# Performance work log

Hardware: AMD Instinct MI355X
Metric: run time of the kernel (lower is better)

Reference implementation:

```python
import jax, jax.numpy as jnp
import numpy as np

B, S, E = 2, 2048, 2048
H, KVH, D = 16, 4, 128
GROUPS = H // KVH
WINDOW = 1024
CAP = 50.0
ROPE_BASE = 10000.0
RMS_EPS = 1e-6
LN_EPS = 1e-5

def setup_inputs() -> dict:
    key = jax.random.key(0)
    ks = jax.random.split(key, 5)
    return {
        "x": jax.random.normal(ks[0], (B, S, E), jnp.float32),
        "Wq": jax.random.normal(ks[1], (E, E), jnp.float32) * (1.0 / np.sqrt(E)),
        "Wk": jax.random.normal(ks[2], (KVH * D, E), jnp.float32) * (1.0 / np.sqrt(E)),
        "Wv": jax.random.normal(ks[3], (KVH * D, E), jnp.float32) * (1.0 / np.sqrt(E)),
        "Wo": jax.random.normal(ks[4], (E, E), jnp.float32) * (1.0 / np.sqrt(E * H)),
        "q_norm_w": jnp.ones((D,), jnp.float32),
        "k_norm_w": jnp.ones((D,), jnp.float32),
        "ln_gamma": jnp.ones((E,), jnp.float32),
        "ln_beta": jnp.zeros((E,), jnp.float32),
    }

def _rmsnorm(t, w):
    # normalize over last (head) dim
    var = jnp.mean(jnp.square(t), axis=-1, keepdims=True)
    return t * jax.lax.rsqrt(var + RMS_EPS) * w

def _rope(t):
    # t: [B, h, S, D]; rotate-half RoPE
    half = D // 2
    inv_freq = 1.0 / (ROPE_BASE ** (jnp.arange(0, D, 2, dtype=jnp.float32) / D))  # [D/2]
    ang = jnp.arange(S, dtype=jnp.float32)[:, None] * inv_freq[None, :]  # [S, D/2]
    cos = jnp.concatenate([jnp.cos(ang), jnp.cos(ang)], axis=-1)  # [S, D]
    sin = jnp.concatenate([jnp.sin(ang), jnp.sin(ang)], axis=-1)
    t1, t2 = t[..., :half], t[..., half:]
    rot = jnp.concatenate([-t2, t1], axis=-1)
    return t * cos + rot * sin

def reference(x, Wq, Wk, Wv, Wo, q_norm_w, k_norm_w, ln_gamma, ln_beta):
    b, s, _ = x.shape
    q = (x @ Wq.T).reshape(b, s, H, D).transpose(0, 2, 1, 3)    # [B,H,S,D]
    k = (x @ Wk.T).reshape(b, s, KVH, D).transpose(0, 2, 1, 3)  # [B,KVH,S,D]
    v = (x @ Wv.T).reshape(b, s, KVH, D).transpose(0, 2, 1, 3)
    # QK-RMSNorm (Gemma/PaLM2 style), then RoPE
    q = _rope(_rmsnorm(q, q_norm_w))
    k = _rope(_rmsnorm(k, k_norm_w))
    # GQA: repeat KV heads to match query heads
    k = jnp.repeat(k, GROUPS, axis=1)  # [B,H,S,D]
    v = jnp.repeat(v, GROUPS, axis=1)
    scores = jnp.einsum('bhqd,bhkd->bhqk', q, k) / jnp.sqrt(jnp.asarray(D, x.dtype))
    # tanh logit softcap (Gemma2)
    scores = CAP * jnp.tanh(scores / CAP)
    # causal + sliding-window mask: attend to j with 0 <= i-j < WINDOW
    i = jnp.arange(s)[:, None]
    j = jnp.arange(s)[None, :]
    mask = (j <= i) & ((i - j) < WINDOW)  # [S,S]
    neg = jnp.finfo(scores.dtype).min
    scores = jnp.where(mask[None, None], scores, neg)
    attn = jax.nn.softmax(scores, axis=-1)
    out = jnp.einsum('bhqk,bhkd->bhqd', attn, v)  # [B,H,S,D]
    out = out.transpose(0, 2, 1, 3).reshape(b, s, E) @ Wo.T
    # residual + LayerNorm (post-norm)
    y = x + out
    mu = jnp.mean(y, axis=-1, keepdims=True)
    var = jnp.var(y, axis=-1, keepdims=True)
    return (y - mu) * jax.lax.rsqrt(var + LN_EPS) * ln_gamma + ln_beta
```

## Files before the change

### kernel.cpp

```cpp
#include <hip/hip_runtime.h>
#include <stdint.h>

typedef __attribute__((ext_vector_type(8))) short short8;
typedef __attribute__((ext_vector_type(4))) float f32x4;
typedef unsigned short u16;
typedef unsigned int u32;

#define NTOK 4096
#define E 2048
#define S 2048
#define NH 16
#define NKVH 4
#define HD 128
#define NQKV 3072

__device__ __forceinline__ float bf2f(u16 u) {
    return __uint_as_float(((u32)u) << 16);
}
__device__ __forceinline__ u16 f2bf(float f) {
    u32 u = __float_as_uint(f);
    u32 r = (u + 0x7fffu + ((u >> 16) & 1u)) >> 16;
    return (u16)r;
}
__device__ __forceinline__ void gload_lds16(const u16* g, u16* l) {
    __builtin_amdgcn_global_load_lds(
        (const __attribute__((address_space(1))) unsigned int*)(g),
        (__attribute__((address_space(3))) unsigned int*)(l), 16, 0, 0);
}

__global__ void cast5(const float* __restrict__ x, const float* __restrict__ wq,
                      const float* __restrict__ wk, const float* __restrict__ wv,
                      const float* __restrict__ wo,
                      u16* __restrict__ xb, u16* __restrict__ wqkvb,
                      u16* __restrict__ wob) {
    int i = blockIdx.x * 256 + threadIdx.x;
    const float* s; u16* d; int rel;
    if (i < 2097152)      { s = x;  d = xb;  rel = i; }
    else if (i < 3145728) { s = wq; d = wqkvb; rel = i - 2097152; }
    else if (i < 3407872) { s = wk; d = wqkvb + 4194304; rel = i - 3145728; }
    else if (i < 3670016) { s = wv; d = wqkvb + 5242880; rel = i - 3407872; }
    else                  { s = wo; d = wob; rel = i - 3670016; }
    float4 v = *(const float4*)(s + (size_t)rel * 4);
    ushort4 o;
    o.x = f2bf(v.x); o.y = f2bf(v.y); o.z = f2bf(v.z); o.w = f2bf(v.w);
    *(ushort4*)(d + (size_t)rel * 4) = o;
}

#define LADDR(row, ko) ((row) * 64 + ((ko) ^ (((row) & 7) << 3)))

__device__ __forceinline__ void stageA(u16* lds, const u16* g, int ldsrow0,
                                       int g0, int g1, int kt, int K, int tid) {
    const int rr = tid >> 3;
    const int chunk = (tid & 7) ^ (rr & 7);
    const int w8 = (tid >> 6) * 8;
    gload_lds16(g + (size_t)(g0 + rr) * K + kt + chunk * 8,
                lds + (ldsrow0 + w8) * 64);
    gload_lds16(g + (size_t)(g1 + rr) * K + kt + chunk * 8,
                lds + (ldsrow0 + 64 + w8) * 64);
}
__device__ __forceinline__ void stageB(u16* lds, const u16* g, int ldsrow0,
                                       int b0, int b1, int kt, int K, int tid) {
    const int rr = tid >> 3;
    const int grow = (rr & 31) | ((rr & 32) << 1);
    const int chunk = (tid & 7) ^ (rr & 7);
    const int w8 = (tid >> 6) * 8;
    gload_lds16(g + (size_t)(b0 + grow) * K + kt + chunk * 8,
                lds + (ldsrow0 + w8) * 64);
    gload_lds16(g + (size_t)(b1 + grow) * K + kt + chunk * 8,
                lds + (ldsrow0 + 64 + w8) * 64);
}

#define GSB   __builtin_amdgcn_sched_barrier(0)
#define GBAR  __builtin_amdgcn_s_barrier()
#define LGKM0 do { asm volatile("s_waitcnt lgkmcnt(0)" ::: "memory"); GSB; } while (0)
#define MIDBAR do { GSB; GBAR; LGKM0; } while (0)
#define ENDBAR do { __builtin_amdgcn_s_setprio(0); GSB; GBAR; } while (0)

__global__ __launch_bounds__(512, 2)
void gemm8p(const u16* __restrict__ A, const u16* __restrict__ Bt,
            float* __restrict__ C, int M, int N, int K) {
    __shared__ u16 As[2 * 16384];
    __shared__ u16 Bs[2 * 16384];
    const int tid = threadIdx.x;
    const int w = tid >> 6, lane = tid & 63;
    const int lr = lane & 15, quad = lane >> 4;
    const int qo = quad * 8;
    const int wm = (w >> 2) * 128, wn = (w & 3) * 64;
    const int wmh = (w >> 2) * 64, wnq = (w & 3) * 32;

    const int nbx = N >> 8;
    int wg = blockIdx.x;
    {
        const int nwg = gridDim.x;
        const int q = nwg >> 3, r = nwg & 7;
        const int xcd = wg & 7, loc = wg >> 3;
        wg = (xcd < r ? xcd * (q + 1) : r * (q + 1) + (xcd - r) * q) + loc;
    }
    const int n0 = (wg % nbx) << 8;
    const int m0 = (wg / nbx) << 8;

    const u16* gA = A + (size_t)m0 * K;
    const u16* gB = Bt + (size_t)n0 * K;
    const int nt = K >> 6;

    f32x4 acc[8][4];
#pragma unroll
    for (int mi = 0; mi < 8; mi++)
#pragma unroll
        for (int ni = 0; ni < 4; ni++)
            acc[mi][ni] = (f32x4){0.f, 0.f, 0.f, 0.f};

    short8 alo[4][2], ahi[4][2], blo[2][2], bhi[2][2];

    stageA(As, gA, 0, 0, 128, 0, K, tid);
    stageB(Bs, gB, 0, 0, 128, 0, K, tid);
    stageB(Bs, gB, 128, 32, 160, 0, K, tid);
    stageA(As, gA, 128, 64, 192, 0, K, tid);
    if (nt > 1) {
        stageA(As + 16384, gA, 0, 0, 128, 64, K, tid);
        stageB(Bs + 16384, gB, 0, 0, 128, 64, K, tid);
        stageB(Bs + 16384, gB, 128, 32, 160, 64, K, tid);
        asm volatile("s_waitcnt vmcnt(6)" ::: "memory");
    } else {
        asm volatile("s_waitcnt vmcnt(0)" ::: "memory");
    }
    GSB; GBAR;

    for (int t = 0; t < nt; ++t) {
        const int pb = t & 1;
        u16* Ap = As + pb * 16384;
        u16* Bp = Bs + pb * 16384;
        u16* An = As + (pb ^ 1) * 16384;
        const int kt1 = (t + 1) << 6, kt2 = (t + 2) << 6;

#pragma unroll
        for (int mi = 0; mi < 4; mi++)
#pragma unroll
            for (int kk = 0; kk < 2; kk++)
                alo[mi][kk] = *(const short8*)&Ap[LADDR(wmh + mi * 16 + lr, kk * 32 + qo)];
#pragma unroll
        for (int ni = 0; ni < 2; ni++)
#pragma unroll
            for (int kk = 0; kk < 2; kk++)
                blo[ni][kk] = *(const short8*)&Bp[LADDR(wnq + ni * 16 + lr, kk * 32 + qo)];
        if (t + 1 < nt) stageA(An, gA, 128, 64, 192, kt1, K, tid);
        MIDBAR;
        __builtin_amdgcn_s_setprio(1);
#pragma unroll
        for (int mi = 0; mi < 4; mi++)
#pragma unroll
            for (int ni = 0; ni < 2; ni++)
#pragma unroll
                for (int kk = 0; kk < 2; kk++)
                    acc[mi][ni] = __builtin_amdgcn_mfma_f32_16x16x32_bf16(
                        alo[mi][kk], blo[ni][kk], acc[mi][ni], 0, 0, 0);
        ENDBAR;

#pragma unroll
        for (int ni = 0; ni < 2; ni++)
#pragma unroll
            for (int kk = 0; kk < 2; kk++)
                bhi[ni][kk] = *(const short8*)&Bp[LADDR(128 + wnq + ni * 16 + lr, kk * 32 + qo)];
        if (t + 2 < nt) stageA(Ap, gA, 0, 0, 128, kt2, K, tid);
        MIDBAR;
        __builtin_amdgcn_s_setprio(1);
#pragma unroll
        for (int mi = 0; mi < 4; mi++)
#pragma unroll
            for (int ni = 0; ni < 2; ni++)
#pragma unroll
                for (int kk = 0; kk < 2; kk++)
                    acc[mi][ni + 2] = __builtin_amdgcn_mfma_f32_16x16x32_bf16(
                        alo[mi][kk], bhi[ni][kk], acc[mi][ni + 2], 0, 0, 0);
        ENDBAR;

#pragma unroll
        for (int mi = 0; mi < 4; mi++)
#pragma unroll
            for (int kk = 0; kk < 2; kk++)
                ahi[mi][kk] = *(const short8*)&Ap[LADDR(128 + wmh + mi * 16 + lr, kk * 32 + qo)];
        if (t + 2 < nt) stageB(Bp, gB, 0, 0, 128, kt2, K, tid);
        MIDBAR;
        __builtin_amdgcn_s_setprio(1);
#pragma unroll
        for (int mi = 0; mi < 4; mi++)
#pragma unroll
            for (int ni = 0; ni < 2; ni++)
#pragma unroll
                for (int kk = 0; kk < 2; kk++)
                    acc[mi + 4][ni + 2] = __builtin_amdgcn_mfma_f32_16x16x32_bf16(
                        ahi[mi][kk], bhi[ni][kk], acc[mi + 4][ni + 2], 0, 0, 0);
        ENDBAR;

        if (t + 2 < nt) stageB(Bp, gB, 128, 32, 160, kt2, K, tid);
        __builtin_amdgcn_s_setprio(1);
#pragma unroll
        for (int mi = 0; mi < 4; mi++)
#pragma unroll
            for (int ni = 0; ni < 2; ni++)
#pragma unroll
                for (int kk = 0; kk < 2; kk++)
                    acc[mi + 4][ni] = __builtin_amdgcn_mfma_f32_16x16x32_bf16(
                        ahi[mi][kk], blo[ni][kk], acc[mi + 4][ni], 0, 0, 0);
        __builtin_amdgcn_s_setprio(0);
        if (t + 2 >= nt) {
            asm volatile("s_waitcnt vmcnt(0)" ::: "memory");
        } else {
            asm volatile("s_waitcnt vmcnt(6)" ::: "memory");
        }
        GSB; GBAR;
    }

#pragma unroll
    for (int mi = 0; mi < 8; mi++)
#pragma unroll
        for (int ni = 0; ni < 4; ni++) {
            const int row = m0 + wm + mi * 16 + quad * 4;
            const int col = n0 + wn + ni * 16 + lr;
            f32x4 v = acc[mi][ni];
            C[(size_t)(row + 0) * N + col] = v[0];
            C[(size_t)(row + 1) * N + col] = v[1];
            C[(size_t)(row + 2) * N + col] = v[2];
            C[(size_t)(row + 3) * N + col] = v[3];
        }
}

__global__ __launch_bounds__(256)
void rmsrope2(const float* __restrict__ qkv,
              const float* __restrict__ qw, const float* __restrict__ kw,
              u16* __restrict__ qdst, u16* __restrict__ kdst) {
    int p = blockIdx.x * 4 + (threadIdx.x >> 6);
    int lane = threadIdx.x & 63;
    const float* src; const float* w; u16* dst; int HH;
    if (p < NTOK * NH) { src = qkv; w = qw; dst = qdst; HH = NH; }
    else { p -= NTOK * NH; src = qkv + 2048; w = kw; dst = kdst; HH = NKVH; }
    int n = p / HH;
    int h = p - n * HH;
    int b = n >> 11;
    int s = n & 2047;
    const float* row = src + (size_t)n * NQKV + h * HD;
    float t1 = row[lane];
    float t2 = row[lane + 64];
    float ss = t1 * t1 + t2 * t2;
#pragma unroll
    for (int o = 1; o < 64; o <<= 1) ss += __shfl_xor(ss, o);
    float r = rsqrtf(ss * (1.f / 128.f) + 1e-6f);
    float a1 = t1 * r * w[lane];
    float a2 = t2 * r * w[lane + 64];
    float freq = expf(lane * -0.14391156831212787f);
    float ang = (float)s * freq;
    float sn, cs;
    sincosf(ang, &sn, &cs);
    float o1 = a1 * cs - a2 * sn;
    float o2 = a2 * cs + a1 * sn;
    size_t base = (((size_t)(b * HH + h)) * S + s) * HD;
    dst[base + lane] = f2bf(o1);
    dst[base + 64 + lane] = f2bf(o2);
}

#define LDT 65
__global__ __launch_bounds__(256)
void vtrans(const float* __restrict__ src, u16* __restrict__ dst) {
    __shared__ u16 Ts[128 * LDT];
    const int t = threadIdx.x;
    const int s0 = blockIdx.x * 64;
    const int kh = blockIdx.y;
    const int b = blockIdx.z;
    const float* base = src + ((size_t)(b * S + s0)) * NQKV + 2560 + kh * HD;
#pragma unroll
    for (int i = 0; i < 8; i++) {
        int idx = i * 256 + t;
        int r = idx >> 5, c4 = (idx & 31) * 4;
        float4 v = *(const float4*)(base + (size_t)r * NQKV + c4);
        Ts[(c4 + 0) * LDT + r] = f2bf(v.x);
        Ts[(c4 + 1) * LDT + r] = f2bf(v.y);
        Ts[(c4 + 2) * LDT + r] = f2bf(v.z);
        Ts[(c4 + 3) * LDT + r] = f2bf(v.w);
    }
    __syncthreads();
    u16* obase = dst + ((size_t)(b * NKVH + kh) * HD) * S + s0;
#pragma unroll
    for (int i = 0; i < 4; i++) {
        int idx = i * 256 + t;
        int d = idx >> 3, s8 = (idx & 7) * 8;
        const u16* row = &Ts[d * LDT + s8];
        short8 o;
#pragma unroll
        for (int j = 0; j < 8; j++) o[j] = (short)row[j];
        *(short8*)(obase + (size_t)d * S + s8) = o;
    }
}

#define KSX(key, cb) ((key) * 128 + ((((cb) ^ ((key) & 15))) * 8))
#define VSX(d, cb)   ((d) * 64 + ((((cb) ^ ((d) & 7))) * 8))
#define PSX(row, cb) ((row) * 64 + ((((cb) ^ ((row) & 7))) * 8))
#define QBLK 64

__global__ __launch_bounds__(256, 4)
void attn_mfma(const u16* __restrict__ qa, const u16* __restrict__ ka,
               const u16* __restrict__ vt, u16* __restrict__ out) {
    __shared__ u16 Ks[64 * 128];
    __shared__ u16 Vs[128 * 64];
    __shared__ u16 Ps[64 * 64];
    const int tid = threadIdx.x;
    const int w = tid >> 6, lane = tid & 63;
    const int lr = lane & 15, quad = lane >> 4;
    const int hb = blockIdx.x;
    const int h = hb >> 1, b = hb & 1;
    const int kh = h >> 2;
    const int qt = (int)(gridDim.y - 1) - blockIdx.y;
    const int q0 = qt * QBLK;
    const int qg0 = q0 + w * 16;

    const float KQK = 0.0051006974f;
    const float KP  = -144.26950408889634f;

    short8 qf[4];
    {
        const u16* qrow = qa + (((size_t)(b * NH + h)) * S + qg0 + lr) * HD;
#pragma unroll
        for (int c = 0; c < 4; c++)
            qf[c] = *(const short8*)(qrow + c * 32 + quad * 8);
    }

    f32x4 O[8];
#pragma unroll
    for (int dt = 0; dt < 8; dt++) O[dt] = (f32x4){0.f, 0.f, 0.f, 0.f};
    float l[4] = {0.f, 0.f, 0.f, 0.f};

    const u16* kbase0 = ka + (((size_t)(b * NKVH + kh)) * S) * HD;
    const u16* vtbase0 = vt + ((size_t)(b * NKVH + kh) * HD) * S;

    const int jt0 = (q0 >= 1024) ? (q0 - 1024) : 0;
    const int jtend = q0;
    const int qmin = qg0, qmax = qg0 + 15;

    for (int jt = jt0; jt <= jtend; jt += 64) {
        const u16* kbase = kbase0 + (size_t)jt * HD;
        const u16* vtbase = vtbase0 + jt;
        __syncthreads();
#pragma unroll
        for (int i = 0; i < 4; i++) {
            int idx = i * 256 + tid;
            int key = idx >> 4, cbk = (idx & 15) ^ (key & 15);
            gload_lds16(kbase + (size_t)key * HD + cbk * 8,
                        &Ks[(i * 256 + w * 64) * 8]);
            int dd = idx >> 3, cbv = (idx & 7) ^ (dd & 7);
            gload_lds16(vtbase + (size_t)dd * S + cbv * 8,
                        &Vs[(i * 256 + w * 64) * 8]);
        }
        __syncthreads();

        u16* Pw = &Ps[w * 16 * 64];
        bool any = false;

#pragma unroll
        for (int kt = 0; kt < 4; kt++) {
            const int keymin = jt + kt * 16;
            bool need = (keymin <= qmax) && (keymin + 15 >= qmin - 1023);
            bool full = (keymin + 15 <= qmin) && (keymin >= qmax - 1023);
            if (need) {
                any = true;
                f32x4 a = (f32x4){0.f, 0.f, 0.f, 0.f};
#pragma unroll
                for (int c = 0; c < 4; c++) {
                    short8 kf = *(const short8*)(&Ks[KSX(kt * 16 + lr, 4 * c + quad)]);
                    a = __builtin_amdgcn_mfma_f32_16x16x32_bf16(qf[c], kf, a, 0, 0, 0);
                }
#pragma unroll
                for (int r = 0; r < 4; r++) {
                    float t = __builtin_amdgcn_exp2f(a[r] * KQK);
                    float p = __builtin_amdgcn_exp2f(
                        KP * __builtin_amdgcn_rcpf(t + 1.f));
                    if (!full) {
                        int rel = keymin + lr - (qg0 + quad * 4 + r);
                        bool valid = (rel <= 0) && (rel > -1024);
                        p = valid ? p : 0.f;
                    }
                    l[r] += p;
                    Pw[PSX(quad * 4 + r, kt * 2 + (lr >> 3)) + (lr & 7)] =
                        (u16)(__float_as_uint(p) >> 16);
                }
            } else {
#pragma unroll
                for (int r = 0; r < 4; r++)
                    Pw[PSX(quad * 4 + r, kt * 2 + (lr >> 3)) + (lr & 7)] = 0;
            }
        }

        if (any) {
#pragma unroll
            for (int c2 = 0; c2 < 2; c2++) {
                short8 pf = *(const short8*)(&Pw[PSX(lr, c2 * 4 + quad)]);
#pragma unroll
                for (int dt = 0; dt < 8; dt++) {
                    short8 vf = *(const short8*)(&Vs[VSX(dt * 16 + lr, c2 * 4 + quad)]);
                    O[dt] = __builtin_amdgcn_mfma_f32_16x16x32_bf16(pf, vf, O[dt], 0, 0, 0);
                }
            }
        }
    }

#pragma unroll
    for (int r = 0; r < 4; r++) {
        l[r] += __shfl_xor(l[r], 1);
        l[r] += __shfl_xor(l[r], 2);
        l[r] += __shfl_xor(l[r], 4);
        l[r] += __shfl_xor(l[r], 8);
    }
#pragma unroll
    for (int r = 0; r < 4; r++) {
        float inv = 1.f / l[r];
        u16* orow = out + ((size_t)(b * S + qg0 + quad * 4 + r)) * E + h * HD;
#pragma unroll
        for (int dt = 0; dt < 8; dt++)
            orow[dt * 16 + lr] = f2bf(O[dt][r] * inv);
    }
}

__global__ __launch_bounds__(256)
void ln_kernel(const float* __restrict__ x, const float* __restrict__ pr,
               const float* __restrict__ g, const float* __restrict__ be,
               float* __restrict__ out) {
    int n = blockIdx.x;
    int tid = threadIdx.x;
    const float* xr = x + (size_t)n * E;
    const float* p = pr + (size_t)n * E;
    float y[8];
    float s = 0.f, ss = 0.f;
#pragma unroll
    for (int i = 0; i < 2; i++) {
        float4 a = *(const float4*)(xr + tid * 8 + i * 4);
        float4 b = *(const float4*)(p + tid * 8 + i * 4);
        float v0 = a.x + b.x, v1 = a.y + b.y, v2 = a.z + b.z, v3 = a.w + b.w;
        y[i * 4 + 0] = v0; y[i * 4 + 1] = v1; y[i * 4 + 2] = v2; y[i * 4 + 3] = v3;
        s += v0 + v1 + v2 + v3;
        ss += v0 * v0 + v1 * v1 + v2 * v2 + v3 * v3;
    }
#pragma unroll
    for (int o = 1; o < 64; o <<= 1) {
        s += __shfl_xor(s, o);
        ss += __shfl_xor(ss, o);
    }
    __shared__ float r0[4], r1[4];
    int w = tid >> 6;
    if ((tid & 63) == 0) { r0[w] = s; r1[w] = ss; }
    __syncthreads();
    s = r0[0] + r0[1] + r0[2] + r0[3];
    ss = r1[0] + r1[1] + r1[2] + r1[3];
    float mu = s * (1.f / 2048.f);
    float var = ss * (1.f / 2048.f) - mu * mu;
    float rs = rsqrtf(var + 1e-5f);
    float* orow = out + (size_t)n * E;
#pragma unroll
    for (int i = 0; i < 8; i++) {
        int c = tid * 8 + i;
        orow[c] = (y[i] - mu) * rs * g[c] + be[c];
    }
}

extern "C" void kernel_launch(void* const* d_in, const int* in_sizes, int n_in,
                              void* d_out, int out_size, void* d_ws, size_t ws_size,
                              hipStream_t stream) {
    (void)in_sizes; (void)n_in; (void)out_size; (void)ws_size;
    const float* x   = (const float*)d_in[0];
    const float* Wq  = (const float*)d_in[1];
    const float* Wk  = (const float*)d_in[2];
    const float* Wv  = (const float*)d_in[3];
    const float* Wo  = (const float*)d_in[4];
    const float* qnw = (const float*)d_in[5];
    const float* knw = (const float*)d_in[6];
    const float* lng = (const float*)d_in[7];
    const float* lnb = (const float*)d_in[8];
    float* out = (float*)d_out;

    char* ws = (char*)d_ws;
    size_t off = 0;
    auto alloc = [&](size_t bytes) -> char* {
        char* pp = ws + off;
        off = (off + bytes + 255) & ~(size_t)255;
        return pp;
    };
    u16*  xb     = (u16*)alloc((size_t)NTOK * E * 2);
    u16*  Wqkvb  = (u16*)alloc((size_t)NQKV * E * 2);
    u16*  Wob    = (u16*)alloc((size_t)E * E * 2);
    float* qkvraw= (float*)alloc((size_t)NTOK * NQKV * 4);
    u16*  qaa    = (u16*)alloc((size_t)NTOK * E * 2);
    u16*  kaa    = (u16*)alloc((size_t)NTOK * 512 * 2);
    u16*  vtt    = (u16*)alloc((size_t)NTOK * 512 * 2);
    u16*  attn_o = xb;
    float* proj  = qkvraw;

    cast5<<<dim3(18432), 256, 0, stream>>>(x, Wq, Wk, Wv, Wo, xb, Wqkvb, Wob);

    gemm8p<<<dim3((NTOK / 256) * (NQKV / 256)), 512, 0, stream>>>(
        xb, Wqkvb, qkvraw, NTOK, NQKV, E);

    rmsrope2<<<dim3((NTOK * NH + NTOK * NKVH) / 4), 256, 0, stream>>>(
        qkvraw, qnw, knw, qaa, kaa);
    vtrans<<<dim3(S / 64, NKVH, 2), 256, 0, stream>>>(qkvraw, vtt);

    attn_mfma<<<dim3(NH * 2, S / QBLK), 256, 0, stream>>>(qaa, kaa, vtt, attn_o);

    gemm8p<<<dim3((NTOK / 256) * (E / 256)), 512, 0, stream>>>(
        attn_o, Wob, proj, NTOK, E, E);

    ln_kernel<<<dim3(NTOK), 256, 0, stream>>>(x, proj, lng, lnb, out);
}
```

Baseline: 339.6 us.

## Split-K the output projection GEMM and merge rmsrope/vtrans into one launch

The output projection GEMM (4096x2048x2048) is split along K into two halves, doubling the grid from 128 to 256 workgroups so that more of the device's compute units are occupied. The two partial results are written to separate buffers and summed in the LayerNorm kernel, which now reads an extra fp32 matrix. Separately, the RMSNorm+RoPE and V-transpose kernels are fused into a single launch, dispatched by block index, to save one launch. The trade-off is extra global traffic for the second partial buffer, and the fused kernel now reserves transpose shared memory for every block.

```diff
diff --git a/kernel.cpp b/kernel.cpp
--- a/kernel.cpp
+++ b/kernel.cpp
@@ -78,7 +78,7 @@
 
 __global__ __launch_bounds__(512, 2)
 void gemm8p(const u16* __restrict__ A, const u16* __restrict__ Bt,
-            float* __restrict__ C, int M, int N, int K) {
+            float* __restrict__ C, int M, int N, int K, int ksz, int nsplit) {
     __shared__ u16 As[2 * 16384];
     __shared__ u16 Bs[2 * 16384];
     const int tid = threadIdx.x;
@@ -96,12 +96,15 @@
         const int xcd = wg & 7, loc = wg >> 3;
         wg = (xcd < r ? xcd * (q + 1) : r * (q + 1) + (xcd - r) * q) + loc;
     }
+    int split = 0;
+    if (nsplit == 2) { split = wg & 1; wg >>= 1; }
     const int n0 = (wg % nbx) << 8;
     const int m0 = (wg / nbx) << 8;
 
-    const u16* gA = A + (size_t)m0 * K;
-    const u16* gB = Bt + (size_t)n0 * K;
-    const int nt = K >> 6;
+    const u16* gA = A + (size_t)m0 * K + split * ksz;
+    const u16* gB = Bt + (size_t)n0 * K + split * ksz;
+    C += (size_t)split * M * N;
+    const int nt = ksz >> 6;
 
     f32x4 acc[8][4];
 #pragma unroll
@@ -225,69 +228,70 @@
         }
 }
 
+#define LDT 65
+#define RMSBLKS 20480
 __global__ __launch_bounds__(256)
-void rmsrope2(const float* __restrict__ qkv,
-              const float* __restrict__ qw, const float* __restrict__ kw,
-              u16* __restrict__ qdst, u16* __restrict__ kdst) {
-    int p = blockIdx.x * 4 + (threadIdx.x >> 6);
-    int lane = threadIdx.x & 63;
-    const float* src; const float* w; u16* dst; int HH;
-    if (p < NTOK * NH) { src = qkv; w = qw; dst = qdst; HH = NH; }
-    else { p -= NTOK * NH; src = qkv + 2048; w = kw; dst = kdst; HH = NKVH; }
-    int n = p / HH;
-    int h = p - n * HH;
-    int b = n >> 11;
-    int s = n & 2047;
-    const float* row = src + (size_t)n * NQKV + h * HD;
-    float t1 = row[lane];
-    float t2 = row[lane + 64];
-    float ss = t1 * t1 + t2 * t2;
-#pragma unroll
-    for (int o = 1; o < 64; o <<= 1) ss += __shfl_xor(ss, o);
-    float r = rsqrtf(ss * (1.f / 128.f) + 1e-6f);
-    float a1 = t1 * r * w[lane];
-    float a2 = t2 * r * w[lane + 64];
-    float freq = expf(lane * -0.14391156831212787f);
-    float ang = (float)s * freq;
-    float sn, cs;
-    sincosf(ang, &sn, &cs);
-    float o1 = a1 * cs - a2 * sn;
-    float o2 = a2 * cs + a1 * sn;
-    size_t base = (((size_t)(b * HH + h)) * S + s) * HD;
-    dst[base + lane] = f2bf(o1);
-    dst[base + 64 + lane] = f2bf(o2);
-}
-
-#define LDT 65
-__global__ __launch_bounds__(256)
-void vtrans(const float* __restrict__ src, u16* __restrict__ dst) {
+void prep(const float* __restrict__ qkv,
+          const float* __restrict__ qw, const float* __restrict__ kw,
+          u16* __restrict__ qdst, u16* __restrict__ kdst, u16* __restrict__ vdst) {
     __shared__ u16 Ts[128 * LDT];
-    const int t = threadIdx.x;
-    const int s0 = blockIdx.x * 64;
-    const int kh = blockIdx.y;
-    const int b = blockIdx.z;
-    const float* base = src + ((size_t)(b * S + s0)) * NQKV + 2560 + kh * HD;
-#pragma unroll
-    for (int i = 0; i < 8; i++) {
-        int idx = i * 256 + t;
-        int r = idx >> 5, c4 = (idx & 31) * 4;
-        float4 v = *(const float4*)(base + (size_t)r * NQKV + c4);
-        Ts[(c4 + 0) * LDT + r] = f2bf(v.x);
-        Ts[(c4 + 1) * LDT + r] = f2bf(v.y);
-        Ts[(c4 + 2) * LDT + r] = f2bf(v.z);
-        Ts[(c4 + 3) * LDT + r] = f2bf(v.w);
-    }
-    __syncthreads();
-    u16* obase = dst + ((size_t)(b * NKVH + kh) * HD) * S + s0;
-#pragma unroll
-    for (int i = 0; i < 4; i++) {
-        int idx = i * 256 + t;
-        int d = idx >> 3, s8 = (idx & 7) * 8;
-        const u16* row = &Ts[d * LDT + s8];
-        short8 o;
-#pragma unroll
-        for (int j = 0; j < 8; j++) o[j] = (short)row[j];
-        *(short8*)(obase + (size_t)d * S + s8) = o;
+    if (blockIdx.x < RMSBLKS) {
+        int p = blockIdx.x * 4 + (threadIdx.x >> 6);
+        int lane = threadIdx.x & 63;
+        const float* src; const float* w; u16* dst; int HH;
+        if (p < NTOK * NH) { src = qkv; w = qw; dst = qdst; HH = NH; }
+        else { p -= NTOK * NH; src = qkv + 2048; w = kw; dst = kdst; HH = NKVH; }
+        int n = p / HH;
+        int h = p - n * HH;
+        int b = n >> 11;
+        int s = n & 2047;
+        const float* row = src + (size_t)n * NQKV + h * HD;
+        float t1 = row[lane];
+        float t2 = row[lane + 64];
+        float ss = t1 * t1 + t2 * t2;
+#pragma unroll
+        for (int o = 1; o < 64; o <<= 1) ss += __shfl_xor(ss, o);
+        float r = rsqrtf(ss * (1.f / 128.f) + 1e-6f);
+        float a1 = t1 * r * w[lane];
+        float a2 = t2 * r * w[lane + 64];
+        float freq = expf(lane * -0.14391156831212787f);
+        float ang = (float)s * freq;
+        float sn, cs;
+        sincosf(ang, &sn, &cs);
+        float o1 = a1 * cs - a2 * sn;
+        float o2 = a2 * cs + a1 * sn;
+        size_t base = (((size_t)(b * HH + h)) * S + s) * HD;
+        dst[base + lane] = f2bf(o1);
+        dst[base + 64 + lane] = f2bf(o2);
+    } else {
+        const int idx = blockIdx.x - RMSBLKS;
+        const int t = threadIdx.x;
+        const int s0 = (idx & 31) * 64;
+        const int kh = (idx >> 5) & 3;
+        const int b = idx >> 7;
+        const float* base = qkv + ((size_t)(b * S + s0)) * NQKV + 2560 + kh * HD;
+#pragma unroll
+        for (int i = 0; i < 8; i++) {
+            int ii = i * 256 + t;
+            int r = ii >> 5, c4 = (ii & 31) * 4;
+            float4 v = *(const float4*)(base + (size_t)r * NQKV + c4);
+            Ts[(c4 + 0) * LDT + r] = f2bf(v.x);
+            Ts[(c4 + 1) * LDT + r] = f2bf(v.y);
+            Ts[(c4 + 2) * LDT + r] = f2bf(v.z);
+            Ts[(c4 + 3) * LDT + r] = f2bf(v.w);
+        }
+        __syncthreads();
+        u16* obase = vdst + ((size_t)(b * NKVH + kh) * HD) * S + s0;
+#pragma unroll
+        for (int i = 0; i < 4; i++) {
+            int ii = i * 256 + t;
+            int d = ii >> 3, s8 = (ii & 7) * 8;
+            const u16* row = &Ts[d * LDT + s8];
+            short8 o;
+#pragma unroll
+            for (int j = 0; j < 8; j++) o[j] = (short)row[j];
+            *(short8*)(obase + (size_t)d * S + s8) = o;
+        }
     }
 }
 
@@ -420,19 +424,25 @@
 
 __global__ __launch_bounds__(256)
 void ln_kernel(const float* __restrict__ x, const float* __restrict__ pr,
+               const float* __restrict__ pr2,
                const float* __restrict__ g, const float* __restrict__ be,
                float* __restrict__ out) {
     int n = blockIdx.x;
     int tid = threadIdx.x;
     const float* xr = x + (size_t)n * E;
     const float* p = pr + (size_t)n * E;
+    const float* p2 = pr2 + (size_t)n * E;
     float y[8];
     float s = 0.f, ss = 0.f;
 #pragma unroll
     for (int i = 0; i < 2; i++) {
         float4 a = *(const float4*)(xr + tid * 8 + i * 4);
         float4 b = *(const float4*)(p + tid * 8 + i * 4);
-        float v0 = a.x + b.x, v1 = a.y + b.y, v2 = a.z + b.z, v3 = a.w + b.w;
+        float c = 0.f;
+        float4 cc = *(const float4*)(p2 + tid * 8 + i * 4);
+        (void)c;
+        float v0 = a.x + b.x + cc.x, v1 = a.y + b.y + cc.y;
+        float v2 = a.z + b.z + cc.z, v3 = a.w + b.w + cc.w;
         y[i * 4 + 0] = v0; y[i * 4 + 1] = v1; y[i * 4 + 2] = v2; y[i * 4 + 3] = v3;
         s += v0 + v1 + v2 + v3;
         ss += v0 * v0 + v1 * v1 + v2 * v2 + v3 * v3;
@@ -494,16 +504,15 @@
     cast5<<<dim3(18432), 256, 0, stream>>>(x, Wq, Wk, Wv, Wo, xb, Wqkvb, Wob);
 
     gemm8p<<<dim3((NTOK / 256) * (NQKV / 256)), 512, 0, stream>>>(
-        xb, Wqkvb, qkvraw, NTOK, NQKV, E);
-
-    rmsrope2<<<dim3((NTOK * NH + NTOK * NKVH) / 4), 256, 0, stream>>>(
-        qkvraw, qnw, knw, qaa, kaa);
-    vtrans<<<dim3(S / 64, NKVH, 2), 256, 0, stream>>>(qkvraw, vtt);
+        xb, Wqkvb, qkvraw, NTOK, NQKV, E, E, 1);
+
+    prep<<<dim3(RMSBLKS + 256), 256, 0, stream>>>(qkvraw, qnw, knw, qaa, kaa, vtt);
 
     attn_mfma<<<dim3(NH * 2, S / QBLK), 256, 0, stream>>>(qaa, kaa, vtt, attn_o);
 
-    gemm8p<<<dim3((NTOK / 256) * (E / 256)), 512, 0, stream>>>(
-        attn_o, Wob, proj, NTOK, E, E);
-
-    ln_kernel<<<dim3(NTOK), 256, 0, stream>>>(x, proj, lng, lnb, out);
-}
+    gemm8p<<<dim3((NTOK / 256) * (E / 256) * 2), 512, 0, stream>>>(
+        attn_o, Wob, proj, NTOK, E, E, E / 2, 2);
+
+    ln_kernel<<<dim3(NTOK), 256, 0, stream>>>(
+        x, proj, proj + (size_t)NTOK * E, lng, lnb, out);
+}
```

Measured after the change: 316.6 us. -6.8%, faster.
